# Optimization experiments

Hardware: AMD Instinct MI355X
Metric: run time of the kernel (lower is better)

## Reference

```python
import jax, jax.numpy as jnp
import numpy as np

B, T, PAST, HID = 2, 512, 4096, 4096
HQ, HKV, D = 32, 8, 128
HH_SIZE, RECENT = 512, 512
CACHE = HH_SIZE + RECENT
MAX_POS = PAST + T


def rotate_half(x):
    h = x.shape[-1] // 2
    return jnp.concatenate([-x[..., h:], x[..., :h]], axis=-1)


def setup_inputs() -> dict:
    key = jax.random.key(0)
    ks = jax.random.split(key, 9)
    hidden_states = jax.random.normal(ks[0], (B, T, HID), jnp.float32) * 0.02
    past_k = jax.random.normal(ks[1], (B, HKV, PAST, D), jnp.float32)
    past_v = jax.random.normal(ks[2], (B, HKV, PAST, D), jnp.float32)
    # accumulated heavy-hitter scores are nonnegative attention-mass sums
    hh_prev = jax.random.uniform(ks[3], (B, HKV, PAST), jnp.float32) * float(T)
    wq = jax.random.normal(ks[4], (HID, HQ * D), jnp.float32) * 0.02
    wk = jax.random.normal(ks[5], (HID, HKV * D), jnp.float32) * 0.02
    wv = jax.random.normal(ks[6], (HID, HKV * D), jnp.float32) * 0.02
    wo = jax.random.normal(ks[7], (HQ * D, HID), jnp.float32) * 0.02
    # RoPE tables [1, MAX_POS, D]
    inv_freq = 1.0 / (10000.0 ** (jnp.arange(0, D, 2, dtype=jnp.float32) / D))
    t = jnp.arange(MAX_POS, dtype=jnp.float32)
    freqs = jnp.einsum('t,f->tf', t, inv_freq)
    emb = jnp.concatenate([freqs, freqs], axis=-1)
    cos = jnp.cos(emb)[None]
    sin = jnp.sin(emb)[None]
    position_ids = jnp.broadcast_to(PAST + jnp.arange(T, dtype=jnp.int32)[None, :], (B, T))
    return {"hidden_states": hidden_states, "past_k": past_k, "past_v": past_v,
            "hh_prev": hh_prev, "wq": wq, "wk": wk, "wv": wv, "wo": wo,
            "cos": cos, "sin": sin, "position_ids": position_ids}


def reference(hidden_states, past_k, past_v, hh_prev, wq, wk, wv, wo, cos, sin, position_ids):
    b, t, _ = hidden_states.shape
    # projections -> [B, H, T, D]
    q = (hidden_states @ wq).reshape(b, t, HQ, D).transpose(0, 2, 1, 3)
    k_new = (hidden_states @ wk).reshape(b, t, HKV, D).transpose(0, 2, 1, 3)
    v_new = (hidden_states @ wv).reshape(b, t, HKV, D).transpose(0, 2, 1, 3)
    # RoPE: gather cos/sin at position_ids -> [B, 1, T, D]
    cos_g = cos[0][position_ids][:, None]
    sin_g = sin[0][position_ids][:, None]
    q = q * cos_g + rotate_half(q) * sin_g
    k_new = k_new * cos_g + rotate_half(k_new) * sin_g
    k = jnp.concatenate([past_k, k_new], axis=2)   # [B, HKV, S, D]
    v = jnp.concatenate([past_v, v_new], axis=2)
    s = k.shape[2]
    past_len = s - t
    g = HQ // HKV
    k_rep = jnp.repeat(k, g, axis=1)               # repeat_interleave over heads
    v_rep = jnp.repeat(v, g, axis=1)
    scores = jnp.einsum('bhtd,bhsd->bhts', q, k_rep) / jnp.sqrt(jnp.float32(D))
    causal = jnp.arange(s)[None, :] <= (past_len + jnp.arange(t))[:, None]  # [T, S]
    scores = jnp.where(causal[None, None], scores, jnp.finfo(scores.dtype).min)
    attn = jax.nn.softmax(scores, axis=-1)         # [B, HQ, T, S]
    ctx = jnp.einsum('bhts,bhsd->bhtd', attn, v_rep)
    out = ctx.transpose(0, 2, 1, 3).reshape(b, t, HQ * D) @ wo
    # --- H2O heavy-hitter score update ('average' GQA reduction) ---
    sc = attn.sum(axis=2)                          # [B, HQ, S]
    sc = sc.reshape(b, HKV, g, s).mean(axis=2)     # [B, HKV, S]
    hh = sc.at[:, :, :past_len].add(hh_prev)
    # --- eviction: topk heavy hitters outside recent window + recent window ---
    select = hh[:, :, : s - RECENT]
    _, top = jax.lax.top_k(select, HH_SIZE)
    top = jnp.sort(top, axis=-1)
    recent_idx = jnp.broadcast_to(jnp.arange(s - RECENT, s, dtype=top.dtype), (b, HKV, RECENT))
    keep = jnp.concatenate([top, recent_idx], axis=-1)      # [B, HKV, CACHE]
    k_kept = jnp.take_along_axis(k, keep[..., None], axis=2)
    v_kept = jnp.take_along_axis(v, keep[..., None], axis=2)
    hh_new = jnp.take_along_axis(hh, keep, axis=2)
    return out, k_kept, v_kept, hh_new
```

## Files before the change

kernel.cpp:

```cpp
#include <hip/hip_runtime.h>
#include <cstdint>
#include <cstddef>

typedef unsigned short u16;
typedef __attribute__((ext_vector_type(8))) short short8;
typedef __attribute__((ext_vector_type(4))) float floatx4;

static __device__ __forceinline__ u16 f2bf(float f){
  union { float f; uint32_t i; } u; u.f = f;
  uint32_t i = u.i;
  return (u16)((i + 0x7FFFu + ((i >> 16) & 1u)) >> 16);
}

static __device__ __forceinline__ void gload_lds16(const u16* g, u16* l){
  __builtin_amdgcn_global_load_lds(
      (const __attribute__((address_space(1))) uint32_t*)g,
      (__attribute__((address_space(3))) uint32_t*)l, 16, 0, 0);
}

static __device__ __forceinline__ uint32_t cvtpk(float lo, float hi){
  uint32_t r;
  asm("v_cvt_pk_bf16_f32 %0, %1, %2" : "=v"(r) : "v"(lo), "v"(hi));
  return r;
}

struct __align__(8) U16x4 { u16 a,b,c,d; };
union PU { short8 s; uint32_t u[4]; };

__global__ void k_convert(const float* __restrict__ src, u16* __restrict__ dst, int n4){
  int i = blockIdx.x*256 + threadIdx.x;
  if (i >= n4) return;
  float4 v = ((const float4*)src)[i];
  U16x4 o{f2bf(v.x), f2bf(v.y), f2bf(v.z), f2bf(v.w)};
  ((U16x4*)dst)[i] = o;
}

__global__ void k_copy_pastk(const float* __restrict__ pk, u16* __restrict__ kcat){
  int i = blockIdx.x*256 + threadIdx.x;
  int slice = i >> 17;
  int off   = i & 131071;
  float4 v = ((const float4*)pk)[i];
  U16x4 o{f2bf(v.x), f2bf(v.y), f2bf(v.z), f2bf(v.w)};
  ((U16x4*)(kcat + (size_t)slice*(4608*128)))[off] = o;
}

__global__ void k_transpose(const float* __restrict__ src, u16* __restrict__ dst,
                            int lds_, int ldd, size_t sstride, size_t dstride){
  src += (size_t)blockIdx.z * sstride; dst += (size_t)blockIdx.z * dstride;
  __shared__ float tile[32][33];
  int bm = blockIdx.y*32, bn = blockIdx.x*32;
  int tx = threadIdx.x & 31, ty = threadIdx.x >> 5;
  #pragma unroll
  for (int r = 0; r < 32; r += 8)
    tile[r+ty][tx] = src[(size_t)(bm + r + ty)*lds_ + bn + tx];
  __syncthreads();
  #pragma unroll
  for (int r = 0; r < 32; r += 8)
    dst[(size_t)(bn + r + ty)*ldd + bm + tx] = f2bf(tile[tx][r+ty]);
}

__global__ __launch_bounds__(256) void k_gemm_bt(
    const u16* __restrict__ A, const u16* __restrict__ Bt, float* __restrict__ C,
    int N, int Kfull, int kLen, size_t cstride)
{
  __shared__ __align__(16) u16 As[128*64];
  __shared__ __align__(16) u16 Bs[128*64];
  const int tid = threadIdx.x, lane = tid & 63, wave = tid >> 6;
  const int m0 = blockIdx.y*128, n0 = blockIdx.x*128;
  const int kOff = blockIdx.z * kLen;
  C += (size_t)blockIdx.z * cstride;
  const int wr = (wave >> 1)*64, wc = (wave & 1)*64;
  const int srow = tid >> 3, sc8 = tid & 7;
  const int csw = (sc8 ^ (srow & 7)) * 8;
  const u16* ap = A  + (size_t)(m0 + srow)*Kfull + kOff + csw;
  const u16* bp = Bt + (size_t)(n0 + srow)*Kfull + kOff + csw;
  u16* la = As + wave*512;
  u16* lb = Bs + wave*512;
  floatx4 acc[4][4] = {};
  const int nk = kLen >> 6;
  for (int kt = 0; kt < nk; ++kt){
    if (kt) __syncthreads();
    const size_t ko = (size_t)kt*64;
    #pragma unroll
    for (int i = 0; i < 4; ++i){
      gload_lds16(ap + (size_t)i*32*Kfull + ko, la + i*2048);
      gload_lds16(bp + (size_t)i*32*Kfull + ko, lb + i*2048);
    }
    __syncthreads();
    #pragma unroll
    for (int ks = 0; ks < 2; ++ks){
      const int c16 = ks*4 + (lane >> 4);
      short8 af[4], bf[4];
      #pragma unroll
      for (int mi = 0; mi < 4; ++mi){
        const int r = wr + mi*16 + (lane & 15);
        af[mi] = *(const short8*)(As + r*64 + ((c16 ^ (r & 7))*8));
      }
      #pragma unroll
      for (int ni = 0; ni < 4; ++ni){
        const int r = wc + ni*16 + (lane & 15);
        bf[ni] = *(const short8*)(Bs + r*64 + ((c16 ^ (r & 7))*8));
      }
      #pragma unroll
      for (int mi = 0; mi < 4; ++mi)
        #pragma unroll
        for (int ni = 0; ni < 4; ++ni)
          acc[mi][ni] = __builtin_amdgcn_mfma_f32_16x16x32_bf16(af[mi], bf[ni], acc[mi][ni], 0,0,0);
    }
  }
  #pragma unroll
  for (int mi = 0; mi < 4; ++mi)
    #pragma unroll
    for (int ni = 0; ni < 4; ++ni){
      const int col = n0 + wc + ni*16 + (lane & 15);
      const int row = m0 + wr + mi*16 + ((lane >> 4) << 2);
      #pragma unroll
      for (int j = 0; j < 4; ++j)
        C[(size_t)(row + j)*N + col] = acc[mi][ni][j];
    }
}

__global__ void k_add(const float* __restrict__ a, const float* __restrict__ b,
                      float* __restrict__ o, int n4){
  int i = blockIdx.x*256 + threadIdx.x;
  if (i >= n4) return;
  float4 x = ((const float4*)a)[i], y = ((const float4*)b)[i];
  float4 z; z.x=x.x+y.x; z.y=x.y+y.y; z.z=x.z+y.z; z.w=x.w+y.w;
  ((float4*)o)[i] = z;
}

__global__ void k_ctx_combine(const float* __restrict__ a, const float* __restrict__ b,
                              u16* __restrict__ o, int n4){
  int i = blockIdx.x*256 + threadIdx.x;
  if (i >= n4) return;
  float4 x = ((const float4*)a)[i], y = ((const float4*)b)[i];
  U16x4 r{f2bf(x.x+y.x), f2bf(x.y+y.y), f2bf(x.z+y.z), f2bf(x.w+y.w)};
  ((U16x4*)o)[i] = r;
}

__global__ void k_rope_q(const float* __restrict__ qfA, const float* __restrict__ qfB,
                         const float* __restrict__ cosb, const float* __restrict__ sinb,
                         const int* __restrict__ pid, u16* __restrict__ qbo){
  int gid = blockIdx.x*256 + threadIdx.x;
  int d = gid & 63, hh = (gid >> 6) & 31, m = gid >> 11;
  int b = m >> 9, t = m & 511;
  int p = pid[b*512 + t];
  float c = cosb[(size_t)p*128 + d], s = sinb[(size_t)p*128 + d];
  size_t ib = (size_t)m*4096 + hh*128 + d;
  float x = qfA[ib] + qfB[ib], y = qfA[ib+64] + qfB[ib+64];
  const float sc = 0.08838834764831845f;
  size_t ob = (((size_t)(b*32 + hh))*512 + t)*128 + d;
  qbo[ob]      = f2bf((x*c - y*s)*sc);
  qbo[ob + 64] = f2bf((y*c + x*s)*sc);
}

__global__ void k_rope_kv(const float* __restrict__ kvfA, const float* __restrict__ kvfB,
                          const float* __restrict__ cosb, const float* __restrict__ sinb,
                          const int* __restrict__ pid,
                          u16* __restrict__ kcat, u16* __restrict__ vtcat){
  int gid = blockIdx.x*256 + threadIdx.x;
  int d = gid & 63, kv = (gid >> 6) & 7, m = gid >> 9;
  int b = m >> 9, t = m & 511;
  int p = pid[b*512 + t];
  float c = cosb[(size_t)p*128 + d], s = sinb[(size_t)p*128 + d];
  size_t ib = (size_t)m*2048 + kv*128 + d;
  float x = kvfA[ib] + kvfB[ib], y = kvfA[ib+64] + kvfB[ib+64];
  float k0 = x*c - y*s, k1 = y*c + x*s;
  int bk = b*8 + kv;
  size_t kb = ((size_t)bk*4608 + 4096 + t)*128 + d;
  kcat[kb] = f2bf(k0); kcat[kb + 64] = f2bf(k1);
  float v0 = kvfA[ib+1024] + kvfB[ib+1024];
  float v1 = kvfA[ib+1088] + kvfB[ib+1088];
  size_t vb = (size_t)bk*(128*4608) + (size_t)d*4608 + 4096 + t;
  vtcat[vb] = f2bf(v0);
  vtcat[vb + (size_t)64*4608] = f2bf(v1);
}

__global__ __launch_bounds__(256) void k_attn_l(
    const u16* __restrict__ qb, const u16* __restrict__ kcat,
    float* __restrict__ lpart)
{
  __shared__ __align__(16) u16 kl[64*128];
  const int tid = threadIdx.x, lane = tid & 63, wave = tid >> 6;
  const int bid = blockIdx.x;
  const int slice = (bid & 7) + 8*(bid >> 10);
  const int within = (bid >> 3) & 127;
  const int b = slice >> 3, kv = slice & 7;
  const int h = kv*4 + (within >> 5);
  const int tb = (within >> 2) & 7;
  const int sc = within & 3;
  const int t0 = tb*64;
  const int ntiles = 65 + tb;
  const int st0 = sc*18;
  const int st1 = (st0 + 18 < ntiles) ? (st0 + 18) : ntiles;
  const u16* qp = qb + (((size_t)(b*32+h))*512 + t0)*128;
  const u16* kp = kcat + (size_t)slice*(4608*128);

  short8 qf[4];
  {
    const int r = wave*16 + (lane & 15);
    const u16* q0 = qp + (size_t)r*128 + ((lane>>4)*8);
    #pragma unroll
    for (int ks=0; ks<4; ++ks) qf[ks] = *(const short8*)(q0 + ks*32);
  }
  const int c16 = tid & 15, srow = tid >> 4;
  short8 rk[4];
  #pragma unroll
  for (int i=0;i<4;++i)
    rk[i] = *(const short8*)(kp + (size_t)(st0*64 + i*16 + srow)*128 + c16*8);

  float l0=0.f,l1=0.f,l2=0.f,l3=0.f;
  for (int st=st0; st<st1; ++st){
    __syncthreads();
    #pragma unroll
    for (int i=0;i<4;++i){
      const int row = i*16 + srow;
      *(short8*)(kl + row*128 + ((c16 ^ (row&7))*8)) = rk[i];
    }
    __syncthreads();
    if (st+1 < st1){
      #pragma unroll
      for (int i=0;i<4;++i)
        rk[i] = *(const short8*)(kp + (size_t)((st+1)*64 + i*16 + srow)*128 + c16*8);
    }
    floatx4 sacc[4] = {};
    #pragma unroll
    for (int ks=0; ks<4; ++ks){
      const int cc = ks*4 + (lane>>4);
      #pragma unroll
      for (int nf=0; nf<4; ++nf){
        const int r = nf*16 + (lane&15);
        short8 kf = *(const short8*)(kl + r*128 + ((cc ^ (r&7))*8));
        sacc[nf] = __builtin_amdgcn_mfma_f32_16x16x32_bf16(qf[ks], kf, sacc[nf], 0,0,0);
      }
    }
    const bool lastt = (st == ntiles-1);
    #pragma unroll
    for (int nf=0;nf<4;++nf)
      #pragma unroll
      for (int j=0;j<4;++j){
        float e = __expf(sacc[nf][j]);
        if (lastt){
          int scol = nf*16 + (lane&15);
          int tloc = wave*16 + ((lane>>4)<<2) + j;
          if (scol > tloc) e = 0.f;
        }
        if(j==0)l0+=e; else if(j==1)l1+=e; else if(j==2)l2+=e; else l3+=e;
      }
  }
  #pragma unroll
  for (int m=1; m<=8; m<<=1){
    l0 += __shfl_xor(l0,m); l1 += __shfl_xor(l1,m);
    l2 += __shfl_xor(l2,m); l3 += __shfl_xor(l3,m);
  }
  if ((lane & 15) == 0){
    float* lp = lpart + ((((size_t)(b*32+h))*8 + tb)<<8) + (sc<<6) + wave*16 + ((lane>>4)<<2);
    lp[0]=l0; lp[1]=l1; lp[2]=l2; lp[3]=l3;
  }
}

__global__ __launch_bounds__(256) void k_attn_pv(
    const u16* __restrict__ qb, const u16* __restrict__ kcat,
    const u16* __restrict__ vtcat, const float* __restrict__ lpart,
    float* __restrict__ ctxp, float* __restrict__ part)
{
  __shared__ __align__(16) u16 kl[64*128];
  __shared__ __align__(16) u16 vl[128*64];
  __shared__ __align__(16) float plds[64*68];
  __shared__ float cw[4*64];

  const int tid=threadIdx.x, lane=tid&63, wave=tid>>6;
  const int bid=blockIdx.x;
  const int slice = (bid&7) + 8*((bid>>3)>>6);
  const int within = (bid>>3)&63;
  const int b=slice>>3, kv=slice&7;
  const int h  = kv*4 + (within>>4);
  const int tb = (within>>1)&7;
  const int hlf = within&1;
  const int t0 = tb*64;
  const int ntiles = 65+tb;
  const int st0 = hlf ? 33 : 0;
  const int st1 = hlf ? ntiles : 33;
  const u16* qp = qb + (((size_t)(b*32+h))*512 + t0)*128;
  const u16* kp = kcat + (size_t)slice*(4608*128);
  const u16* vp = vtcat + (size_t)slice*(128*4608);
  float* pb = part + (((size_t)(b*32+h))*8 + tb)*4608;
  float* cp = ctxp + (size_t)hlf*4194304;

  float rl[4];
  {
    const float* lp = lpart + ((((size_t)(b*32+h))*8 + tb)<<8);
    const int r0 = wave*16 + ((lane>>4)<<2);
    #pragma unroll
    for (int j=0;j<4;++j){
      int r = r0 + j;
      float l = lp[r] + lp[64+r] + lp[128+r] + lp[192+r];
      rl[j] = 1.f/l;
    }
  }
  short8 qf[4];
  {
    const int r = wave*16 + (lane & 15);
    const u16* q0 = qp + (size_t)r*128 + ((lane>>4)*8);
    #pragma unroll
    for (int ks=0; ks<4; ++ks) qf[ks] = *(const short8*)(q0 + ks*32);
  }
  const int c16 = tid&15, srow = tid>>4;
  const int vc = tid&7,  vrow = tid>>3;
  short8 rk[4], rv[4];
  #pragma unroll
  for (int i=0;i<4;++i){
    rk[i] = *(const short8*)(kp + (size_t)(st0*64 + i*16 + srow)*128 + c16*8);
    rv[i] = *(const short8*)(vp + (size_t)(i*32 + vrow)*4608 + st0*64 + vc*8);
  }
  floatx4 pacc[8] = {};
  const int prow = wave*16 + (lane&15);

  for (int st=st0; st<st1; ++st){
    const int s0 = st*64;
    __syncthreads();
    if (st > st0 && tid < 64)
      pb[s0-64+tid] = cw[tid] + cw[64+tid] + cw[128+tid] + cw[192+tid];
    #pragma unroll
    for (int i=0;i<4;++i){
      const int row = i*16 + srow;
      *(short8*)(kl + row*128 + ((c16 ^ (row&7))*8)) = rk[i];
      const int vr = i*32 + vrow;
      *(short8*)(vl + vr*64 + ((vc ^ (vr&7))*8)) = rv[i];
    }
    __syncthreads();
    if (st+1 < st1){
      #pragma unroll
      for (int i=0;i<4;++i){
        rk[i] = *(const short8*)(kp + (size_t)((st+1)*64 + i*16 + srow)*128 + c16*8);
        rv[i] = *(const short8*)(vp + (size_t)(i*32 + vrow)*4608 + (st+1)*64 + vc*8);
      }
    }
    floatx4 sacc[4] = {};
    #pragma unroll
    for (int ks=0; ks<4; ++ks){
      const int cc = ks*4 + (lane>>4);
      #pragma unroll
      for (int nf=0; nf<4; ++nf){
        const int r = nf*16 + (lane&15);
        short8 kf = *(const short8*)(kl + r*128 + ((cc ^ (r&7))*8));
        sacc[nf] = __builtin_amdgcn_mfma_f32_16x16x32_bf16(qf[ks], kf, sacc[nf], 0,0,0);
      }
    }
    const bool lastt = (st==ntiles-1);
    float cs0=0.f, cs1=0.f, cs2=0.f, cs3=0.f;
    #pragma unroll
    for (int nf=0;nf<4;++nf){
      float cpart=0.f;
      #pragma unroll
      for (int j=0;j<4;++j){
        float e = __expf(sacc[nf][j]);
        if (lastt){
          int scol = nf*16 + (lane&15);
          int tloc = wave*16 + ((lane>>4)<<2) + j;
          if (scol > tloc) e = 0.f;
        }
        float p = e * rl[j];
        plds[(wave*16 + ((lane>>4)<<2) + j)*68 + nf*16 + (lane&15)] = p;
        cpart += p;
      }
      if(nf==0)cs0=cpart; else if(nf==1)cs1=cpart; else if(nf==2)cs2=cpart; else cs3=cpart;
    }
    cs0 += __shfl_xor(cs0,16); cs0 += __shfl_xor(cs0,32);
    cs1 += __shfl_xor(cs1,16); cs1 += __shfl_xor(cs1,32);
    cs2 += __shfl_xor(cs2,16); cs2 += __shfl_xor(cs2,32);
    cs3 += __shfl_xor(cs3,16); cs3 += __shfl_xor(cs3,32);
    {
      const int nfsel = lane >> 4;
      float v = (nfsel==0)?cs0:(nfsel==1)?cs1:(nfsel==2)?cs2:cs3;
      cw[wave*64 + nfsel*16 + (lane & 15)] = v;
    }
    short8 pa[2];
    #pragma unroll
    for (int k2 = 0; k2 < 2; ++k2){
      const float* pp = plds + prow*68 + k2*32 + ((lane>>4)*8);
      float4 x = *(const float4*)pp;
      float4 y = *(const float4*)(pp + 4);
      PU t;
      t.u[0] = cvtpk(x.x, x.y);
      t.u[1] = cvtpk(x.z, x.w);
      t.u[2] = cvtpk(y.x, y.y);
      t.u[3] = cvtpk(y.z, y.w);
      pa[k2] = t.s;
    }
    #pragma unroll
    for (int nf = 0; nf < 8; ++nf){
      const int rv2 = nf*16 + (lane & 15);
      #pragma unroll
      for (int k2 = 0; k2 < 2; ++k2){
        const int c = ((k2*4 + (lane>>4)) ^ (rv2 & 7));
        short8 vf = *(const short8*)(vl + rv2*64 + c*8);
        pacc[nf] = __builtin_amdgcn_mfma_f32_16x16x32_bf16(pa[k2], vf, pacc[nf], 0,0,0);
      }
    }
  }
  __syncthreads();
  if (tid < 64)
    pb[(st1-1)*64 + tid] = cw[tid] + cw[64+tid] + cw[128+tid] + cw[192+tid];
  #pragma unroll
  for (int nf = 0; nf < 8; ++nf)
    #pragma unroll
    for (int j = 0; j < 4; ++j){
      const int trow = t0 + wave*16 + ((lane>>4)<<2) + j;
      const int col  = h*128 + nf*16 + (lane & 15);
      cp[(size_t)(b*512 + trow)*4096 + col] = pacc[nf][j];
    }
}

__global__ void k_hh_reduce(const float* __restrict__ part, const float* __restrict__ hhprev,
                            float* __restrict__ hh){
  int gid = blockIdx.x*256 + threadIdx.x;
  if (gid >= 73728) return;
  int s = gid % 4608; int bk = gid / 4608; int b = bk >> 3, kv = bk & 7;
  float acc = 0.f;
  #pragma unroll
  for (int h4 = 0; h4 < 4; ++h4){
    const float* pp = part + (((size_t)(b*32 + kv*4 + h4))*8)*4608 + s;
    #pragma unroll
    for (int tbb = 0; tbb < 8; ++tbb)
      if (s < 4160 + tbb*64) acc += pp[(size_t)tbb*4608];
  }
  acc *= 0.25f;
  if (s < 4096) acc += hhprev[(size_t)bk*4096 + s];
  hh[gid] = acc;
}

__global__ __launch_bounds__(256) void k_topk(const float* __restrict__ hh, int* __restrict__ keep,
                                              float* __restrict__ hh_new){
  __shared__ uint64_t keys[4096];
  __shared__ int hist[256];
  __shared__ int tsum[256];
  __shared__ uint64_t sprefix;
  __shared__ int srank;
  const int bk = blockIdx.x, tid = threadIdx.x;
  const float* hp = hh + (size_t)bk*4608;
  for (int i = tid; i < 4096; i += 256){
    uint32_t vb = __float_as_uint(hp[i]);
    keys[i] = ((uint64_t)(0xFFFFFFFFu - vb) << 12) | (uint32_t)i;
  }
  if (tid == 0){ sprefix = 0; srank = 512; }
  __syncthreads();
  for (int shift = 40; shift >= 0; shift -= 8){
    hist[tid] = 0;
    __syncthreads();
    const uint64_t pref = sprefix;
    const uint64_t hm = ~((1ull << (shift+8)) - 1ull);
    for (int i = tid; i < 4096; i += 256){
      uint64_t k = keys[i];
      if ((k & hm) == pref) atomicAdd(&hist[(int)((k >> shift) & 255)], 1);
    }
    __syncthreads();
    if (tid == 0){
      int r = srank, b = 0;
      for (;;){ int c = hist[b]; if (r <= c) break; r -= c; ++b; }
      srank = r; sprefix = pref | ((uint64_t)b << shift);
    }
    __syncthreads();
  }
  const uint64_t kstar = sprefix;
  const int base = tid*16;
  int cnt = 0;
  #pragma unroll
  for (int j = 0; j < 16; ++j) cnt += (keys[base+j] <= kstar) ? 1 : 0;
  tsum[tid] = cnt;
  __syncthreads();
  for (int off = 1; off < 256; off <<= 1){
    int v = (tid >= off) ? tsum[tid-off] : 0;
    __syncthreads();
    tsum[tid] += v;
    __syncthreads();
  }
  int pos = tsum[tid] - cnt;
  for (int j = 0; j < 16; ++j){
    uint64_t k = keys[base+j];
    if (k <= kstar){
      keep[bk*1024 + pos] = base + j;
      hh_new[(size_t)bk*1024 + pos] = __uint_as_float(0xFFFFFFFFu - (uint32_t)(k >> 12));
      ++pos;
    }
  }
  for (int i = tid; i < 512; i += 256){
    keep[bk*1024 + 512 + i] = 4096 + i;
    hh_new[(size_t)bk*1024 + 512 + i] = hp[4096 + i];
  }
}

__global__ void k_gather(const float* __restrict__ pastk, const float* __restrict__ pastv,
                         const float* __restrict__ kvfA, const float* __restrict__ kvfB,
                         const float* __restrict__ cosb, const float* __restrict__ sinb,
                         const int* __restrict__ pid, const int* __restrict__ keep,
                         float* __restrict__ outk, float* __restrict__ outv){
  int r = blockIdx.x*2 + (threadIdx.x >> 7);
  int d = threadIdx.x & 127;
  int bk = r >> 10, i = r & 1023;
  int idx = keep[bk*1024 + i];
  float kval, vval;
  if (idx < 4096){
    kval = pastk[((size_t)bk*4096 + idx)*128 + d];
    vval = pastv[((size_t)bk*4096 + idx)*128 + d];
  } else {
    int t = idx - 4096; int b = bk >> 3, kv = bk & 7;
    size_t base = ((size_t)(b*512 + t))*2048 + kv*128;
    int dp = (d < 64) ? d + 64 : d - 64;
    float x  = kvfA[base + d]  + kvfB[base + d];
    float xp = kvfA[base + dp] + kvfB[base + dp];
    int p = pid[b*512 + t];
    float c = cosb[(size_t)p*128 + d], s = sinb[(size_t)p*128 + d];
    kval = x*c + xp*((d < 64) ? -s : s);
    vval = kvfA[base + 1024 + d] + kvfB[base + 1024 + d];
  }
  outk[(size_t)r*128 + d] = kval;
  outv[(size_t)r*128 + d] = vval;
}

extern "C" void kernel_launch(void* const* d_in, const int* in_sizes, int n_in,
                              void* d_out, int out_size, void* d_ws, size_t ws_size,
                              hipStream_t stream){
  const float* hs     = (const float*)d_in[0];
  const float* pastk  = (const float*)d_in[1];
  const float* pastv  = (const float*)d_in[2];
  const float* hhprev = (const float*)d_in[3];
  const float* wq     = (const float*)d_in[4];
  const float* wk     = (const float*)d_in[5];
  const float* wv     = (const float*)d_in[6];
  const float* wo     = (const float*)d_in[7];
  const float* cosb   = (const float*)d_in[8];
  const float* sinb   = (const float*)d_in[9];
  const int*   pid    = (const int*)d_in[10];
  float* out = (float*)d_out;
  char* ws = (char*)d_ws;

  u16*   hsb  = (u16*)(ws + 0);
  u16*   wqt  = (u16*)(ws + 8388608);
  u16*   wkvt = (u16*)(ws + 41943040);
  float* qfA  = (float*)(ws + 58720256);
  float* qfB  = (float*)(ws + 75497472);
  float* kvfA = (float*)(ws + 92274688);
  float* kvfB = (float*)(ws + 100663296);
  u16*   qb   = (u16*)(ws + 109051904);
  u16*   kcat = (u16*)(ws + 117440512);
  u16*   vtc  = (u16*)(ws + 136314880);
  u16*   ctxb = (u16*)(ws + 155189248);
  float* part = (float*)(ws + 163577856);
  float* lprt = (float*)(ws + 173015040);
  float* hhb  = (float*)(ws + 173539328);
  int*   keep = (int*)(ws + 173834240);

  (void)in_sizes; (void)n_in; (void)out_size; (void)ws_size;

  k_convert<<<4096,256,0,stream>>>(hs, hsb, 1048576);
  k_transpose<<<dim3(128,128,1),256,0,stream>>>(wq, wqt, 4096, 4096, 0, 0);
  k_transpose<<<dim3(32,128,1),256,0,stream>>>(wk, wkvt, 1024, 4096, 0, 0);
  k_transpose<<<dim3(32,128,1),256,0,stream>>>(wv, wkvt + (size_t)1024*4096, 1024, 4096, 0, 0);
  k_transpose<<<dim3(4,128,16),256,0,stream>>>(pastv, vtc, 128, 4608,
                                               (size_t)4096*128, (size_t)128*4608);
  k_copy_pastk<<<8192,256,0,stream>>>(pastk, kcat);

  k_gemm_bt<<<dim3(32,8,2),256,0,stream>>>(hsb, wqt, qfA, 4096, 4096, 2048, (size_t)1024*4096);
  k_gemm_bt<<<dim3(16,8,2),256,0,stream>>>(hsb, wkvt, kvfA, 2048, 4096, 2048, (size_t)1024*2048);
  k_transpose<<<dim3(128,128,1),256,0,stream>>>(wo, wqt, 4096, 4096, 0, 0);

  k_rope_q<<<8192,256,0,stream>>>(qfA, qfB, cosb, sinb, pid, qb);
  k_rope_kv<<<2048,256,0,stream>>>(kvfA, kvfB, cosb, sinb, pid, kcat, vtc);

  k_attn_l<<<2048,256,0,stream>>>(qb, kcat, lprt);
  k_attn_pv<<<1024,256,0,stream>>>(qb, kcat, vtc, lprt, qfA, part);
  k_ctx_combine<<<4096,256,0,stream>>>(qfA, qfB, ctxb, 1048576);

  k_gemm_bt<<<dim3(32,8,2),256,0,stream>>>(ctxb, wqt, qfA, 4096, 4096, 2048, (size_t)1024*4096);
  k_add<<<4096,256,0,stream>>>(qfA, qfB, out, 1048576);

  k_hh_reduce<<<288,256,0,stream>>>(part, hhprev, hhb);
  k_topk<<<16,256,0,stream>>>(hhb, keep, out + 8388608);
  k_gather<<<8192,256,0,stream>>>(pastk, pastv, kvfA, kvfB, cosb, sinb, pid, keep,
                                  out + 4194304, out + 6291456);
}
```

Before: 725.6 us.

## Load K/V MFMA fragments directly from global memory instead of LDS staging

Both attention kernels drop the shared-memory K and V tiles and their register prefetch. Each wave now reads its K and transposed-V MFMA fragments straight from global memory, leaning on the L1/L2 caches. The column-sum scratch buffer is double-buffered, so the PV loop needs only one barrier per tile and the L kernel needs none. This removes LDS stores and reads, barriers and LDS pressure, which may allow higher occupancy. In exchange the four waves in a block fetch the same K/V data redundantly, and load latency is no longer hidden by software prefetch.

```diff
diff --git a/kernel.cpp b/kernel.cpp
--- a/kernel.cpp
+++ b/kernel.cpp
@@ -180,7 +180,6 @@
     const u16* __restrict__ qb, const u16* __restrict__ kcat,
     float* __restrict__ lpart)
 {
-  __shared__ __align__(16) u16 kl[64*128];
   const int tid = threadIdx.x, lane = tid & 63, wave = tid >> 6;
   const int bid = blockIdx.x;
   const int slice = (bid & 7) + 8*(bid >> 10);
@@ -203,34 +202,17 @@
     #pragma unroll
     for (int ks=0; ks<4; ++ks) qf[ks] = *(const short8*)(q0 + ks*32);
   }
-  const int c16 = tid & 15, srow = tid >> 4;
-  short8 rk[4];
-  #pragma unroll
-  for (int i=0;i<4;++i)
-    rk[i] = *(const short8*)(kp + (size_t)(st0*64 + i*16 + srow)*128 + c16*8);
+  const int krow = lane & 15, kg = lane >> 4;
 
   float l0=0.f,l1=0.f,l2=0.f,l3=0.f;
   for (int st=st0; st<st1; ++st){
-    __syncthreads();
-    #pragma unroll
-    for (int i=0;i<4;++i){
-      const int row = i*16 + srow;
-      *(short8*)(kl + row*128 + ((c16 ^ (row&7))*8)) = rk[i];
-    }
-    __syncthreads();
-    if (st+1 < st1){
-      #pragma unroll
-      for (int i=0;i<4;++i)
-        rk[i] = *(const short8*)(kp + (size_t)((st+1)*64 + i*16 + srow)*128 + c16*8);
-    }
+    const u16* kt = kp + (size_t)(st*64)*128;
     floatx4 sacc[4] = {};
     #pragma unroll
     for (int ks=0; ks<4; ++ks){
-      const int cc = ks*4 + (lane>>4);
       #pragma unroll
       for (int nf=0; nf<4; ++nf){
-        const int r = nf*16 + (lane&15);
-        short8 kf = *(const short8*)(kl + r*128 + ((cc ^ (r&7))*8));
+        short8 kf = *(const short8*)(kt + (size_t)(nf*16 + krow)*128 + (ks*4 + kg)*8);
         sacc[nf] = __builtin_amdgcn_mfma_f32_16x16x32_bf16(qf[ks], kf, sacc[nf], 0,0,0);
       }
     }
@@ -264,10 +246,8 @@
     const u16* __restrict__ vtcat, const float* __restrict__ lpart,
     float* __restrict__ ctxp, float* __restrict__ part)
 {
-  __shared__ __align__(16) u16 kl[64*128];
-  __shared__ __align__(16) u16 vl[128*64];
   __shared__ __align__(16) float plds[64*68];
-  __shared__ float cw[4*64];
+  __shared__ float cw[2][256];
 
   const int tid=threadIdx.x, lane=tid&63, wave=tid>>6;
   const int bid=blockIdx.x;
@@ -305,45 +285,25 @@
     #pragma unroll
     for (int ks=0; ks<4; ++ks) qf[ks] = *(const short8*)(q0 + ks*32);
   }
-  const int c16 = tid&15, srow = tid>>4;
-  const int vc = tid&7,  vrow = tid>>3;
-  short8 rk[4], rv[4];
-  #pragma unroll
-  for (int i=0;i<4;++i){
-    rk[i] = *(const short8*)(kp + (size_t)(st0*64 + i*16 + srow)*128 + c16*8);
-    rv[i] = *(const short8*)(vp + (size_t)(i*32 + vrow)*4608 + st0*64 + vc*8);
-  }
+  const int krow = lane & 15, kg = lane >> 4;
   floatx4 pacc[8] = {};
   const int prow = wave*16 + (lane&15);
 
   for (int st=st0; st<st1; ++st){
     const int s0 = st*64;
-    __syncthreads();
-    if (st > st0 && tid < 64)
-      pb[s0-64+tid] = cw[tid] + cw[64+tid] + cw[128+tid] + cw[192+tid];
-    #pragma unroll
-    for (int i=0;i<4;++i){
-      const int row = i*16 + srow;
-      *(short8*)(kl + row*128 + ((c16 ^ (row&7))*8)) = rk[i];
-      const int vr = i*32 + vrow;
-      *(short8*)(vl + vr*64 + ((vc ^ (vr&7))*8)) = rv[i];
-    }
-    __syncthreads();
-    if (st+1 < st1){
-      #pragma unroll
-      for (int i=0;i<4;++i){
-        rk[i] = *(const short8*)(kp + (size_t)((st+1)*64 + i*16 + srow)*128 + c16*8);
-        rv[i] = *(const short8*)(vp + (size_t)(i*32 + vrow)*4608 + (st+1)*64 + vc*8);
-      }
-    }
+    const int cur = (st - st0) & 1;
+    __syncthreads();
+    if (st > st0 && tid < 64){
+      const float* c = cw[cur^1];
+      pb[s0-64+tid] = c[tid] + c[64+tid] + c[128+tid] + c[192+tid];
+    }
+    const u16* kt = kp + (size_t)s0*128;
     floatx4 sacc[4] = {};
     #pragma unroll
     for (int ks=0; ks<4; ++ks){
-      const int cc = ks*4 + (lane>>4);
       #pragma unroll
       for (int nf=0; nf<4; ++nf){
-        const int r = nf*16 + (lane&15);
-        short8 kf = *(const short8*)(kl + r*128 + ((cc ^ (r&7))*8));
+        short8 kf = *(const short8*)(kt + (size_t)(nf*16 + krow)*128 + (ks*4 + kg)*8);
         sacc[nf] = __builtin_amdgcn_mfma_f32_16x16x32_bf16(qf[ks], kf, sacc[nf], 0,0,0);
       }
     }
@@ -373,7 +333,7 @@
     {
       const int nfsel = lane >> 4;
       float v = (nfsel==0)?cs0:(nfsel==1)?cs1:(nfsel==2)?cs2:cs3;
-      cw[wave*64 + nfsel*16 + (lane & 15)] = v;
+      cw[cur][wave*64 + nfsel*16 + (lane & 15)] = v;
     }
     short8 pa[2];
     #pragma unroll
@@ -390,18 +350,19 @@
     }
     #pragma unroll
     for (int nf = 0; nf < 8; ++nf){
-      const int rv2 = nf*16 + (lane & 15);
+      const size_t vrow = (size_t)(nf*16 + krow)*4608 + s0;
       #pragma unroll
       for (int k2 = 0; k2 < 2; ++k2){
-        const int c = ((k2*4 + (lane>>4)) ^ (rv2 & 7));
-        short8 vf = *(const short8*)(vl + rv2*64 + c*8);
+        short8 vf = *(const short8*)(vp + vrow + (k2*4 + kg)*8);
         pacc[nf] = __builtin_amdgcn_mfma_f32_16x16x32_bf16(pa[k2], vf, pacc[nf], 0,0,0);
       }
     }
   }
   __syncthreads();
-  if (tid < 64)
-    pb[(st1-1)*64 + tid] = cw[tid] + cw[64+tid] + cw[128+tid] + cw[192+tid];
+  if (tid < 64){
+    const float* c = cw[(st1-1-st0)&1];
+    pb[(st1-1)*64 + tid] = c[tid] + c[64+tid] + c[128+tid] + c[192+tid];
+  }
   #pragma unroll
   for (int nf = 0; nf < 8; ++nf)
     #pragma unroll
```

Result: slower. 1.564 ms (+115.6%).
